# Kernel optimization log

Measured on AMD Instinct MI355X. Metric: run time of the kernel, lower is better.

## Reference

```python
import jax, jax.numpy as jnp
import numpy as np

B, N, D_MODEL, H = 2, 512, 256, 8
DH, DS, DE = 8, 8, 8          # hyperbolic / spherical / euclidean component dims
HEAD = D_MODEL // H           # 32
HALF = HEAD // 2              # 16 rope frequencies
KAPPA_S = 1.0                 # spherical curvature
EPS = 1e-6


def setup_inputs() -> dict:
    key = jax.random.key(0)
    ks = jax.random.split(key, 10)
    h = jax.random.normal(ks[0], (B, N, D_MODEL), jnp.float32)
    # manifold coords: hyperbolic part inside Poincare ball, spherical part on unit sphere
    xh = 0.3 * jnp.tanh(jax.random.normal(ks[1], (B, N, DH), jnp.float32))
    xs_raw = jax.random.normal(ks[2], (B, N, DS), jnp.float32)
    xs = xs_raw / jnp.linalg.norm(xs_raw, axis=-1, keepdims=True)
    xe = jax.random.normal(ks[3], (B, N, DE), jnp.float32)
    x = jnp.concatenate([xh, xs, xe], axis=-1)
    def lin(k):
        return 0.05 * jax.random.normal(k, (D_MODEL, D_MODEL), jnp.float32)
    inp = dict(
        h=h, x=x,
        Wq=lin(ks[4]), bq=jnp.zeros((D_MODEL,), jnp.float32),
        Wk=lin(ks[5]), bk=jnp.zeros((D_MODEL,), jnp.float32),
        Wv=lin(ks[6]), bv=jnp.zeros((D_MODEL,), jnp.float32),
        Wo=lin(ks[7]), bo=jnp.zeros((D_MODEL,), jnp.float32),
        w_kernel=jnp.ones((H, 3), jnp.float32),   # torch init: ones(num_heads, num_comp)
        beta=jnp.ones((H,), jnp.float32),
        edge_bias=0.1 * jax.random.normal(ks[8], (B, 1, N, N), jnp.float32),
        node_mask=jnp.ones((B, N), bool),
    )
    return inp


def _pairwise_geometry(x):
    """Returns dh (B,N,N), sdot (B,N,N), de2 (B,N,N), dist (B,N,N)."""
    xh, xs, xe = x[..., :DH], x[..., DH:DH + DS], x[..., DH + DS:]
    # hyperbolic: Poincare-ball distance arccosh(1 + 2|a-b|^2 / ((1-|a|^2)(1-|b|^2)))
    dh2_num = jnp.sum((xh[:, :, None, :] - xh[:, None, :, :]) ** 2, -1)
    one_m = 1.0 - jnp.sum(xh * xh, -1)                               # (B,N)
    arg = 1.0 + 2.0 * dh2_num / (one_m[:, :, None] * one_m[:, None, :])
    dh = jnp.arccosh(jnp.maximum(arg, 1.0 + EPS))
    # spherical: arccos of dot (unit vectors); raw dot kept for the kernel term
    sdot = jnp.einsum('bnd,bmd->bnm', xs, xs)
    ds = jnp.arccos(jnp.clip(sdot, -1.0 + EPS, 1.0 - EPS)) / np.sqrt(KAPPA_S)
    # euclidean: squared distance (kernel uses -d^2; product dist uses d^2)
    de2 = jnp.sum((xe[:, :, None, :] - xe[:, None, :, :]) ** 2, -1)
    dist = jnp.sqrt(dh * dh + ds * ds + de2)
    return dh, sdot, de2, dist


def reference(h, x, Wq, bq, Wk, bk, Wv, bv, Wo, bo, w_kernel, beta, edge_bias, node_mask):
    scale = 1.0 / np.sqrt(HEAD)
    rope_freq = jnp.exp(-np.log(10000.0) * jnp.arange(HALF, dtype=jnp.float32) / HALF)

    def heads(t):  # (B,N,D) -> (B,H,N,head)
        return t.reshape(B, N, H, HEAD).transpose(0, 2, 1, 3)

    Q = heads(h @ Wq.T + bq)
    K = heads(h @ Wk.T + bk)
    V = heads(h @ Wv.T + bv)

    dh, sdot, de2, dist = _pairwise_geometry(x)

    # M-RoPE: rotate Q by pairwise angle theta_ij = omega * d_M(x_i, x_j)
    theta = dist[..., None] * rope_freq                  # (B,N,N,half)
    cos_t = jnp.cos(theta)[:, None]                      # (B,1,N,N,half)
    sin_t = jnp.sin(theta)[:, None]
    q1, q2 = Q[..., 0::2], Q[..., 1::2]                  # (B,H,N,half)
    k1, k2 = K[..., 0::2], K[..., 1::2]
    qk_same = q1[:, :, :, None, :] * k1[:, :, None, :, :] + q2[:, :, :, None, :] * k2[:, :, None, :, :]
    qk_cross = q1[:, :, :, None, :] * k2[:, :, None, :, :] - q2[:, :, :, None, :] * k1[:, :, None, :, :]
    attn = (cos_t * qk_same + sin_t * qk_cross).sum(-1) * scale   # (B,H,N,N)

    # geodesic kernel bias: per-component kernels [H:-d_H, S:k*a.b, E:-|a-b|^2]
    kernel_stack = jnp.stack([-dh, KAPPA_S * sdot, -de2], axis=-1)  # (B,N,N,3)
    geo = jnp.einsum('hc,bnmc->bhnm', w_kernel, kernel_stack)
    attn = attn + beta[None, :, None, None] * geo + edge_bias

    attn = jnp.where(node_mask[:, None, None, :], attn, -jnp.inf)
    p = jax.nn.softmax(attn, axis=-1)
    out = jnp.einsum('bhnm,bhmd->bhnd', p, V).transpose(0, 2, 1, 3).reshape(B, N, D_MODEL)
    return out @ Wo.T + bo
```

## Files before the change

kernel.cpp:

```cpp
#include <hip/hip_runtime.h>

#define N_TOK 512
#define NH 8

typedef __attribute__((ext_vector_type(8))) short short8;
typedef __attribute__((ext_vector_type(4))) short short4v;
typedef __attribute__((ext_vector_type(4))) float f32x4;

__device__ __forceinline__ unsigned short f2bf(float f) {
    union { float f; unsigned u; } v; v.f = f;
    return (unsigned short)((v.u + 0x7FFF + ((v.u >> 16) & 1)) >> 16);
}

__global__ __launch_bounds__(256) void gemm_qkv_mfma(
    const float* __restrict__ A, const float* __restrict__ x,
    const float* __restrict__ Wq, const float* __restrict__ Wk, const float* __restrict__ Wv,
    const float* __restrict__ bq, const float* __restrict__ bk, const float* __restrict__ bv,
    float* __restrict__ Qb, float* __restrict__ KT, float* __restrict__ Vb,
    float* __restrict__ xT)
{
    const int bx = blockIdx.x;
    const int t = threadIdx.x;
    if (bx >= 768) {
        int idx = bx - 768;
        int b = idx / 24, k = idx % 24;
        const float* src = x + (size_t)b * 512 * 24 + k;
        float* dst = xT + (size_t)b * 12288 + k * 512;
        for (int j = t; j < 512; j += 256) dst[j] = src[j * 24];
        return;
    }
    const int z = bx >> 8, rem = bx & 255;
    const int m0 = (rem >> 3) * 32, n0 = (rem & 7) * 32;
    const float* W    = (z == 0) ? Wq : (z == 1) ? Wk : Wv;
    const float* bias = (z == 0) ? bq : (z == 1) ? bk : bv;

    __shared__ short As[32][264];
    __shared__ short Ws[32][264];

    #pragma unroll
    for (int r = 0; r < 8; ++r) {
        int idx = t + 256 * r;
        int row = idx >> 6, c4 = (idx & 63) * 4;
        float4 a = *(const float4*)&A[(m0 + row) * 256 + c4];
        short4v pa = {(short)f2bf(a.x), (short)f2bf(a.y), (short)f2bf(a.z), (short)f2bf(a.w)};
        *(short4v*)&As[row][c4] = pa;
        float4 w = *(const float4*)&W[(n0 + row) * 256 + c4];
        short4v pw = {(short)f2bf(w.x), (short)f2bf(w.y), (short)f2bf(w.z), (short)f2bf(w.w)};
        *(short4v*)&Ws[row][c4] = pw;
    }
    __syncthreads();

    const int w = t >> 6, lane = t & 63;
    const int wm = (w >> 1) * 16, wn = (w & 1) * 16;
    const int frow = lane & 15, kq = lane >> 4;

    f32x4 acc = {0.f, 0.f, 0.f, 0.f};
    #pragma unroll
    for (int k0 = 0; k0 < 8; ++k0) {
        short8 af = *(const short8*)&As[wm + frow][k0 * 32 + kq * 8];
        short8 wf = *(const short8*)&Ws[wn + frow][k0 * 32 + kq * 8];
        if (z == 1) acc = __builtin_amdgcn_mfma_f32_16x16x32_bf16(wf, af, acc, 0, 0, 0);
        else        acc = __builtin_amdgcn_mfma_f32_16x16x32_bf16(af, wf, acc, 0, 0, 0);
    }
    const int col = lane & 15, rq = (lane >> 4) * 4;
    if (z == 1) {
        int tok = m0 + wm + col;
        int bb = tok >> 9, jloc = tok & 511;
        #pragma unroll
        for (int r = 0; r < 4; ++r) {
            int d = n0 + wn + rq + r;
            KT[(size_t)bb * 131072 + d * 512 + jloc] = acc[r] + bias[d];
        }
    } else {
        float* C = (z == 0) ? Qb : Vb;
        float bsv = bias[n0 + wn + col];
        #pragma unroll
        for (int r = 0; r < 4; ++r)
            C[(m0 + wm + rq + r) * 256 + n0 + wn + col] = acc[r] + bsv;
    }
}

__global__ __launch_bounds__(512, 4) void attn_kernel(
    const float* __restrict__ Q, const float* __restrict__ KT, const float* __restrict__ V,
    const float* __restrict__ x, const float* __restrict__ xT,
    const float* __restrict__ wker, const float* __restrict__ beta,
    const float* __restrict__ eb, float* __restrict__ Ao)
{
    const int i0 = blockIdx.x * 2;
    const int b  = blockIdx.y;
    const int t  = threadIdx.x;
    const int lane = t & 63;
    const int h = __builtin_amdgcn_readfirstlane(t >> 6);

    __shared__ float csn[16][2][64][4];
    __shared__ float es[2][NH][128];
    __shared__ float gdh[2][128], gsd[2][128], gde[2][128];

    const float* q0p = Q + (size_t)(b * N_TOK + i0) * 256 + h * 32;
    const float* q1p = q0p + 256;
    const float wk0 = wker[h * 3 + 0], wk1 = wker[h * 3 + 1], wk2 = wker[h * 3 + 2];
    const float bet = beta[h];
    const float scale = 0.17677669529663687f;

    const int gjj = t & 127;
    const int gfh = __builtin_amdgcn_readfirstlane((t >> 7) & 1);
    const int gii = __builtin_amdgcn_readfirstlane(t >> 8);
    const float* xi = x + (size_t)(b * N_TOK + i0 + gii) * 24;
    float onemi = 1.0f;
    #pragma unroll
    for (int k = 0; k < 8; ++k) onemi -= xi[k] * xi[k];
    float frq[8];
    #pragma unroll
    for (int r = 0; r < 8; ++r)
        frq[r] = __expf(-0.5756462732485115f * (float)(gfh * 8 + r));

    float dsum[2] = {0.f, 0.f};
    float accv[2][4] = {{0.f,0.f,0.f,0.f},{0.f,0.f,0.f,0.f}};
    const int jsub = lane >> 3, dq = lane & 7;

    auto geom = [&](int tile) {
        const float* xc = xT + (size_t)b * 12288 + tile * 128 + gjj;
        float xv[24];
        #pragma unroll
        for (int k = 0; k < 24; ++k) xv[k] = xc[k * 512];
        float dh2 = 0.f, oj = 0.f, sd = 0.f, de2 = 0.f;
        #pragma unroll
        for (int k = 0; k < 8; ++k) { float d = xi[k] - xv[k]; dh2 += d * d; oj += xv[k] * xv[k]; }
        #pragma unroll
        for (int k = 0; k < 8; ++k) sd += xi[8 + k] * xv[8 + k];
        #pragma unroll
        for (int k = 0; k < 8; ++k) { float d = xi[16 + k] - xv[16 + k]; de2 += d * d; }
        float arg = 1.0f + 2.0f * dh2 / (onemi * (1.0f - oj));
        arg = fmaxf(arg, 1.0f + 1e-6f);
        float dh = __logf(arg + sqrtf(arg * arg - 1.0f));
        float sdc = fminf(fmaxf(sd, -1.0f + 1e-6f), 1.0f - 1e-6f);
        float dsp = acosf(sdc);
        float dist = sqrtf(dh * dh + dsp * dsp + de2);
        if (gfh == 0) { gdh[gii][gjj] = dh; gsd[gii][gjj] = sd; gde[gii][gjj] = de2; }
        #pragma unroll
        for (int r = 0; r < 8; ++r) {
            float sv, cv;
            __sincosf(dist * frq[r], &sv, &cv);
            *(float2*)&csn[gfh * 8 + r][gii][gjj >> 1][(gjj & 1) * 2] = make_float2(cv, sv);
        }
    };

    geom(0);
    __syncthreads();

    for (int tile = 0; tile < 4; ++tile) {
        {
            float dot[2][2] = {{0.f, 0.f}, {0.f, 0.f}};
            #pragma unroll
            for (int fg = 0; fg < 2; ++fg) {
                const float* kp = KT + (size_t)b * 131072 + (h * 32 + fg * 16) * 512
                                + tile * 128 + 2 * lane;
                float2 kv[16];
                #pragma unroll
                for (int cc = 0; cc < 16; ++cc) kv[cc] = *(const float2*)(kp + cc * 512);
                #pragma unroll
                for (int fl = 0; fl < 8; ++fl) {
                    const int f = fg * 8 + fl;
                    float2 k1 = kv[fl * 2], k2 = kv[fl * 2 + 1];
                    float q10 = q0p[f * 2], q20 = q0p[f * 2 + 1];
                    float q11 = q1p[f * 2], q21 = q1p[f * 2 + 1];
                    float4 c0 = *(const float4*)&csn[f][0][lane][0];
                    float4 c1 = *(const float4*)&csn[f][1][lane][0];
                    dot[0][0] += c0.x * (q10 * k1.x + q20 * k2.x) + c0.y * (q10 * k2.x - q20 * k1.x);
                    dot[0][1] += c0.z * (q10 * k1.y + q20 * k2.y) + c0.w * (q10 * k2.y - q20 * k1.y);
                    dot[1][0] += c1.x * (q11 * k1.x + q21 * k2.x) + c1.y * (q11 * k2.x - q21 * k1.x);
                    dot[1][1] += c1.z * (q11 * k1.y + q21 * k2.y) + c1.w * (q11 * k2.y - q21 * k1.y);
                }
            }
            #pragma unroll
            for (int ii = 0; ii < 2; ++ii) {
                float2 g1 = *(const float2*)&gdh[ii][2 * lane];
                float2 g2 = *(const float2*)&gsd[ii][2 * lane];
                float2 g3 = *(const float2*)&gde[ii][2 * lane];
                float2 e2 = *(const float2*)&eb[((size_t)b * N_TOK + i0 + ii) * N_TOK
                                                + tile * 128 + 2 * lane];
                float s0 = dot[ii][0] * scale + bet * (wk1 * g2.x - wk0 * g1.x - wk2 * g3.x) + e2.x;
                float s1 = dot[ii][1] * scale + bet * (wk1 * g2.y - wk0 * g1.y - wk2 * g3.y) + e2.y;
                float e0 = __expf(s0), e1 = __expf(s1);
                dsum[ii] += e0 + e1;
                *(float2*)&es[ii][h][2 * lane] = make_float2(e0, e1);
            }
        }
        __syncthreads();
        {
            const float* vp = V + (size_t)(b * N_TOK + tile * 128 + jsub) * 256 + h * 32 + dq * 4;
            #pragma unroll
            for (int it = 0; it < 16; ++it) {
                float4 v4 = *(const float4*)(vp + it * 8 * 256);
                int j = it * 8 + jsub;
                float e0 = es[0][h][j], e1 = es[1][h][j];
                accv[0][0] += e0 * v4.x; accv[0][1] += e0 * v4.y;
                accv[0][2] += e0 * v4.z; accv[0][3] += e0 * v4.w;
                accv[1][0] += e1 * v4.x; accv[1][1] += e1 * v4.y;
                accv[1][2] += e1 * v4.z; accv[1][3] += e1 * v4.w;
            }
        }
        if (tile < 3) geom(tile + 1);
        __syncthreads();
    }

    #pragma unroll
    for (int ii = 0; ii < 2; ++ii) {
        float v = dsum[ii];
        v += __shfl_xor(v, 1);  v += __shfl_xor(v, 2);  v += __shfl_xor(v, 4);
        v += __shfl_xor(v, 8);  v += __shfl_xor(v, 16); v += __shfl_xor(v, 32);
        dsum[ii] = 1.0f / v;
    }
    #pragma unroll
    for (int ii = 0; ii < 2; ++ii)
        #pragma unroll
        for (int dd = 0; dd < 4; ++dd) {
            float a = accv[ii][dd];
            a += __shfl_xor(a, 8); a += __shfl_xor(a, 16); a += __shfl_xor(a, 32);
            accv[ii][dd] = a;
        }
    if (jsub == 0) {
        #pragma unroll
        for (int ii = 0; ii < 2; ++ii) {
            float4 o;
            o.x = accv[ii][0] * dsum[ii]; o.y = accv[ii][1] * dsum[ii];
            o.z = accv[ii][2] * dsum[ii]; o.w = accv[ii][3] * dsum[ii];
            *(float4*)&Ao[(size_t)(b * N_TOK + i0 + ii) * 256 + h * 32 + dq * 4] = o;
        }
    }
}

__global__ __launch_bounds__(256) void gemm_out_mfma(
    const float* __restrict__ Ao, const float* __restrict__ Wo,
    const float* __restrict__ bo, float* __restrict__ out)
{
    const int t = threadIdx.x;
    const int m0 = (blockIdx.x >> 3) * 32, n0 = (blockIdx.x & 7) * 32;

    __shared__ short As[32][264];
    __shared__ short Ws[32][264];

    #pragma unroll
    for (int r = 0; r < 8; ++r) {
        int idx = t + 256 * r;
        int row = idx >> 6, c4 = (idx & 63) * 4;
        float4 a = *(const float4*)&Ao[(m0 + row) * 256 + c4];
        short4v pa = {(short)f2bf(a.x), (short)f2bf(a.y), (short)f2bf(a.z), (short)f2bf(a.w)};
        *(short4v*)&As[row][c4] = pa;
        float4 w = *(const float4*)&Wo[(n0 + row) * 256 + c4];
        short4v pw = {(short)f2bf(w.x), (short)f2bf(w.y), (short)f2bf(w.z), (short)f2bf(w.w)};
        *(short4v*)&Ws[row][c4] = pw;
    }
    __syncthreads();

    const int w = t >> 6, lane = t & 63;
    const int wm = (w >> 1) * 16, wn = (w & 1) * 16;
    const int frow = lane & 15, kq = lane >> 4;

    f32x4 acc = {0.f, 0.f, 0.f, 0.f};
    #pragma unroll
    for (int k0 = 0; k0 < 8; ++k0) {
        short8 af = *(const short8*)&As[wm + frow][k0 * 32 + kq * 8];
        short8 wf = *(const short8*)&Ws[wn + frow][k0 * 32 + kq * 8];
        acc = __builtin_amdgcn_mfma_f32_16x16x32_bf16(af, wf, acc, 0, 0, 0);
    }
    const int col = lane & 15, rq = (lane >> 4) * 4;
    float bsv = bo[n0 + wn + col];
    #pragma unroll
    for (int r = 0; r < 4; ++r)
        out[(m0 + wm + rq + r) * 256 + n0 + wn + col] = acc[r] + bsv;
}

extern "C" void kernel_launch(void* const* d_in, const int* in_sizes, int n_in,
                              void* d_out, int out_size, void* d_ws, size_t ws_size,
                              hipStream_t stream) {
    const float* hin  = (const float*)d_in[0];
    const float* x    = (const float*)d_in[1];
    const float* Wq   = (const float*)d_in[2];
    const float* bq   = (const float*)d_in[3];
    const float* Wk   = (const float*)d_in[4];
    const float* bk   = (const float*)d_in[5];
    const float* Wv   = (const float*)d_in[6];
    const float* bv   = (const float*)d_in[7];
    const float* Wo   = (const float*)d_in[8];
    const float* bo   = (const float*)d_in[9];
    const float* wker = (const float*)d_in[10];
    const float* beta = (const float*)d_in[11];
    const float* eb   = (const float*)d_in[12];
    float* out = (float*)d_out;
    float* w   = (float*)d_ws;

    float* Qb = w;
    float* KT = w + 262144;
    float* Vb = w + 524288;
    float* Ao = w + 786432;
    float* xT = w + 1048576;

    hipLaunchKernelGGL(gemm_qkv_mfma, dim3(816), dim3(256), 0, stream,
                       hin, x, Wq, Wk, Wv, bq, bk, bv, Qb, KT, Vb, xT);
    hipLaunchKernelGGL(attn_kernel, dim3(256, 2), dim3(512), 0, stream,
                       Qb, KT, Vb, x, xT, wker, beta, eb, Ao);
    hipLaunchKernelGGL(gemm_out_mfma, dim3(256), dim3(256), 0, stream,
                       Ao, Wo, bo, out);
}
```

Measured before the change: 135.0 us.

## Split pairwise geometry into separate kernel and make attention waves independent

Moves the per-pair manifold geometry (dh, sdot, de2, dist) into a new kernel that writes four B×N×N planes to the workspace. The attention kernel becomes wave-independent: each wave handles one (batch, head, row-pair), reads the precomputed geometry and computes its own sin/cos, with no block barriers. K is stored interleaved per frequency so each lane loads one float4. The previous design shared geometry and sincos across 8 heads in a block. Now each head redoes 16 sincos per pair and reads about 8 MB of extra geometry from global memory, trading block synchronisation for more transcendental work and memory traffic.

Result: slower. 138.0 us (+2.2%).

```diff
diff --git a/kernel.cpp b/kernel.cpp
--- a/kernel.cpp
+++ b/kernel.cpp
@@ -13,22 +13,13 @@
 }
 
 __global__ __launch_bounds__(256) void gemm_qkv_mfma(
-    const float* __restrict__ A, const float* __restrict__ x,
+    const float* __restrict__ A,
     const float* __restrict__ Wq, const float* __restrict__ Wk, const float* __restrict__ Wv,
     const float* __restrict__ bq, const float* __restrict__ bk, const float* __restrict__ bv,
-    float* __restrict__ Qb, float* __restrict__ KT, float* __restrict__ Vb,
-    float* __restrict__ xT)
+    float* __restrict__ Qb, float* __restrict__ KR, float* __restrict__ Vb)
 {
     const int bx = blockIdx.x;
     const int t = threadIdx.x;
-    if (bx >= 768) {
-        int idx = bx - 768;
-        int b = idx / 24, k = idx % 24;
-        const float* src = x + (size_t)b * 512 * 24 + k;
-        float* dst = xT + (size_t)b * 12288 + k * 512;
-        for (int j = t; j < 512; j += 256) dst[j] = src[j * 24];
-        return;
-    }
     const int z = bx >> 8, rem = bx & 255;
     const int m0 = (rem >> 3) * 32, n0 = (rem & 7) * 32;
     const float* W    = (z == 0) ? Wq : (z == 1) ? Wk : Wv;
@@ -65,11 +56,12 @@
     const int col = lane & 15, rq = (lane >> 4) * 4;
     if (z == 1) {
         int tok = m0 + wm + col;
-        int bb = tok >> 9, jloc = tok & 511;
+        int bb = tok >> 9, j = tok & 511;
         #pragma unroll
         for (int r = 0; r < 4; ++r) {
             int d = n0 + wn + rq + r;
-            KT[(size_t)bb * 131072 + d * 512 + jloc] = acc[r] + bias[d];
+            int h = d >> 5, dd = d & 31, f = dd >> 1, r2 = dd & 1;
+            KR[((size_t)bb * 128 + h * 16 + f) * 1024 + j * 2 + r2] = acc[r] + bias[d];
         }
     } else {
         float* C = (z == 0) ? Qb : Vb;
@@ -80,128 +72,150 @@
     }
 }
 
-__global__ __launch_bounds__(512, 4) void attn_kernel(
-    const float* __restrict__ Q, const float* __restrict__ KT, const float* __restrict__ V,
-    const float* __restrict__ x, const float* __restrict__ xT,
+__global__ __launch_bounds__(256) void geo_kernel(
+    const float* __restrict__ x, float* __restrict__ geo)
+{
+    const int j0 = blockIdx.x * 256;
+    const int i  = blockIdx.y;
+    const int b  = blockIdx.z;
+    const int t  = threadIdx.x;
+
+    __shared__ float xls[256 * 25];
+    const float4* xsrc = (const float4*)(x + ((size_t)b * N_TOK + j0) * 24);
+    #pragma unroll
+    for (int r = 0; r < 6; ++r) {
+        int idx = t + 256 * r;
+        float4 v = xsrc[idx];
+        int row = idx / 6, c = (idx % 6) * 4;
+        float* dst = &xls[row * 25 + c];
+        dst[0] = v.x; dst[1] = v.y; dst[2] = v.z; dst[3] = v.w;
+    }
+    const float* xi = x + ((size_t)b * N_TOK + i) * 24;
+    float onemi = 1.0f;
+    #pragma unroll
+    for (int k = 0; k < 8; ++k) onemi -= xi[k] * xi[k];
+    __syncthreads();
+
+    const float* xr = &xls[t * 25];
+    float dh2 = 0.f, oj = 0.f, sd = 0.f, de2 = 0.f;
+    #pragma unroll
+    for (int k = 0; k < 8; ++k) { float xj = xr[k]; float d = xi[k] - xj; dh2 += d * d; oj += xj * xj; }
+    #pragma unroll
+    for (int k = 0; k < 8; ++k) sd += xi[8 + k] * xr[8 + k];
+    #pragma unroll
+    for (int k = 0; k < 8; ++k) { float d = xi[16 + k] - xr[16 + k]; de2 += d * d; }
+    float arg = 1.0f + 2.0f * dh2 / (onemi * (1.0f - oj));
+    arg = fmaxf(arg, 1.0f + 1e-6f);
+    float dh = __logf(arg + sqrtf(arg * arg - 1.0f));
+    float sdc = fminf(fmaxf(sd, -1.0f + 1e-6f), 1.0f - 1e-6f);
+    float dsp = acosf(sdc);
+    float dist = sqrtf(dh * dh + dsp * dsp + de2);
+
+    size_t idx = ((size_t)b * N_TOK + i) * N_TOK + j0 + t;
+    geo[idx]               = dh;
+    geo[idx +     524288]  = sd;
+    geo[idx + 2 * 524288]  = de2;
+    geo[idx + 3 * 524288]  = dist;
+}
+
+__global__ __launch_bounds__(256, 4) void attn_kernel(
+    const float* __restrict__ Q, const float* __restrict__ KR, const float* __restrict__ V,
+    const float* __restrict__ geo, const float* __restrict__ eb,
     const float* __restrict__ wker, const float* __restrict__ beta,
-    const float* __restrict__ eb, float* __restrict__ Ao)
+    float* __restrict__ Ao)
 {
-    const int i0 = blockIdx.x * 2;
-    const int b  = blockIdx.y;
-    const int t  = threadIdx.x;
+    const float FRQ[16] = {
+        1.0f, 0.5623413251903491f, 0.31622776601683794f, 0.17782794100389228f,
+        0.1f, 0.05623413251903491f, 0.031622776601683794f, 0.017782794100389228f,
+        0.01f, 0.005623413251903491f, 0.0031622776601683794f, 0.0017782794100389228f,
+        0.001f, 0.0005623413251903491f, 0.00031622776601683795f, 0.00017782794100389228f};
+
+    const int t = threadIdx.x;
     const int lane = t & 63;
-    const int h = __builtin_amdgcn_readfirstlane(t >> 6);
-
-    __shared__ float csn[16][2][64][4];
-    __shared__ float es[2][NH][128];
-    __shared__ float gdh[2][128], gsd[2][128], gde[2][128];
-
-    const float* q0p = Q + (size_t)(b * N_TOK + i0) * 256 + h * 32;
+    const int wv = t >> 6;
+    const int wid = blockIdx.x * 4 + wv;
+    const int b  = __builtin_amdgcn_readfirstlane(wid >> 11);
+    const int h  = __builtin_amdgcn_readfirstlane((wid >> 8) & 7);
+    const int ip = __builtin_amdgcn_readfirstlane(wid & 255);
+    const int i0 = ip * 2;
+
+    __shared__ float es[4][2][128];
+
+    const float* q0p = Q + ((size_t)b * N_TOK + i0) * 256 + h * 32;
     const float* q1p = q0p + 256;
     const float wk0 = wker[h * 3 + 0], wk1 = wker[h * 3 + 1], wk2 = wker[h * 3 + 2];
     const float bet = beta[h];
     const float scale = 0.17677669529663687f;
 
-    const int gjj = t & 127;
-    const int gfh = __builtin_amdgcn_readfirstlane((t >> 7) & 1);
-    const int gii = __builtin_amdgcn_readfirstlane(t >> 8);
-    const float* xi = x + (size_t)(b * N_TOK + i0 + gii) * 24;
-    float onemi = 1.0f;
-    #pragma unroll
-    for (int k = 0; k < 8; ++k) onemi -= xi[k] * xi[k];
-    float frq[8];
-    #pragma unroll
-    for (int r = 0; r < 8; ++r)
-        frq[r] = __expf(-0.5756462732485115f * (float)(gfh * 8 + r));
+    const size_t gbase = ((size_t)b * N_TOK + i0) * N_TOK;
+    const float* kbase = KR + ((size_t)b * 128 + h * 16) * 1024;
 
     float dsum[2] = {0.f, 0.f};
-    float accv[2][4] = {{0.f,0.f,0.f,0.f},{0.f,0.f,0.f,0.f}};
+    float acc[2][4] = {{0.f,0.f,0.f,0.f},{0.f,0.f,0.f,0.f}};
     const int jsub = lane >> 3, dq = lane & 7;
 
-    auto geom = [&](int tile) {
-        const float* xc = xT + (size_t)b * 12288 + tile * 128 + gjj;
-        float xv[24];
-        #pragma unroll
-        for (int k = 0; k < 24; ++k) xv[k] = xc[k * 512];
-        float dh2 = 0.f, oj = 0.f, sd = 0.f, de2 = 0.f;
-        #pragma unroll
-        for (int k = 0; k < 8; ++k) { float d = xi[k] - xv[k]; dh2 += d * d; oj += xv[k] * xv[k]; }
-        #pragma unroll
-        for (int k = 0; k < 8; ++k) sd += xi[8 + k] * xv[8 + k];
-        #pragma unroll
-        for (int k = 0; k < 8; ++k) { float d = xi[16 + k] - xv[16 + k]; de2 += d * d; }
-        float arg = 1.0f + 2.0f * dh2 / (onemi * (1.0f - oj));
-        arg = fmaxf(arg, 1.0f + 1e-6f);
-        float dh = __logf(arg + sqrtf(arg * arg - 1.0f));
-        float sdc = fminf(fmaxf(sd, -1.0f + 1e-6f), 1.0f - 1e-6f);
-        float dsp = acosf(sdc);
-        float dist = sqrtf(dh * dh + dsp * dsp + de2);
-        if (gfh == 0) { gdh[gii][gjj] = dh; gsd[gii][gjj] = sd; gde[gii][gjj] = de2; }
-        #pragma unroll
-        for (int r = 0; r < 8; ++r) {
-            float sv, cv;
-            __sincosf(dist * frq[r], &sv, &cv);
-            *(float2*)&csn[gfh * 8 + r][gii][gjj >> 1][(gjj & 1) * 2] = make_float2(cv, sv);
-        }
-    };
-
-    geom(0);
-    __syncthreads();
-
     for (int tile = 0; tile < 4; ++tile) {
-        {
-            float dot[2][2] = {{0.f, 0.f}, {0.f, 0.f}};
+        const int j0 = tile * 128;
+        float2 gdh[2], gsd[2], gde[2], gds[2];
+        #pragma unroll
+        for (int ii = 0; ii < 2; ++ii) {
+            size_t gi = gbase + (size_t)ii * N_TOK + j0 + 2 * lane;
+            gdh[ii] = *(const float2*)&geo[gi];
+            gsd[ii] = *(const float2*)&geo[gi + 524288];
+            gde[ii] = *(const float2*)&geo[gi + 2 * 524288];
+            gds[ii] = *(const float2*)&geo[gi + 3 * 524288];
+        }
+        float dot[2][2] = {{0.f, 0.f}, {0.f, 0.f}};
+        #pragma unroll
+        for (int fg = 0; fg < 2; ++fg) {
+            float4 kv[8];
             #pragma unroll
-            for (int fg = 0; fg < 2; ++fg) {
-                const float* kp = KT + (size_t)b * 131072 + (h * 32 + fg * 16) * 512
-                                + tile * 128 + 2 * lane;
-                float2 kv[16];
+            for (int fl = 0; fl < 8; ++fl)
+                kv[fl] = *(const float4*)&kbase[(size_t)(fg * 8 + fl) * 1024 + (j0 + 2 * lane) * 2];
+            #pragma unroll
+            for (int fl = 0; fl < 8; ++fl) {
+                const int f = fg * 8 + fl;
+                const float frq = FRQ[f];
+                float4 kk = kv[fl];
                 #pragma unroll
-                for (int cc = 0; cc < 16; ++cc) kv[cc] = *(const float2*)(kp + cc * 512);
-                #pragma unroll
-                for (int fl = 0; fl < 8; ++fl) {
-                    const int f = fg * 8 + fl;
-                    float2 k1 = kv[fl * 2], k2 = kv[fl * 2 + 1];
-                    float q10 = q0p[f * 2], q20 = q0p[f * 2 + 1];
-                    float q11 = q1p[f * 2], q21 = q1p[f * 2 + 1];
-                    float4 c0 = *(const float4*)&csn[f][0][lane][0];
-                    float4 c1 = *(const float4*)&csn[f][1][lane][0];
-                    dot[0][0] += c0.x * (q10 * k1.x + q20 * k2.x) + c0.y * (q10 * k2.x - q20 * k1.x);
-                    dot[0][1] += c0.z * (q10 * k1.y + q20 * k2.y) + c0.w * (q10 * k2.y - q20 * k1.y);
-                    dot[1][0] += c1.x * (q11 * k1.x + q21 * k2.x) + c1.y * (q11 * k2.x - q21 * k1.x);
-                    dot[1][1] += c1.z * (q11 * k1.y + q21 * k2.y) + c1.w * (q11 * k2.y - q21 * k1.y);
+                for (int ii = 0; ii < 2; ++ii) {
+                    const float* qp = ii ? q1p : q0p;
+                    float q1 = qp[f * 2], q2 = qp[f * 2 + 1];
+                    float c0, s0, c1, s1;
+                    __sincosf(gds[ii].x * frq, &s0, &c0);
+                    __sincosf(gds[ii].y * frq, &s1, &c1);
+                    float t1 = q1 * kk.x + q2 * kk.y;
+                    float t2 = q1 * kk.y - q2 * kk.x;
+                    dot[ii][0] += c0 * t1 + s0 * t2;
+                    t1 = q1 * kk.z + q2 * kk.w;
+                    t2 = q1 * kk.w - q2 * kk.z;
+                    dot[ii][1] += c1 * t1 + s1 * t2;
                 }
             }
-            #pragma unroll
-            for (int ii = 0; ii < 2; ++ii) {
-                float2 g1 = *(const float2*)&gdh[ii][2 * lane];
-                float2 g2 = *(const float2*)&gsd[ii][2 * lane];
-                float2 g3 = *(const float2*)&gde[ii][2 * lane];
-                float2 e2 = *(const float2*)&eb[((size_t)b * N_TOK + i0 + ii) * N_TOK
-                                                + tile * 128 + 2 * lane];
-                float s0 = dot[ii][0] * scale + bet * (wk1 * g2.x - wk0 * g1.x - wk2 * g3.x) + e2.x;
-                float s1 = dot[ii][1] * scale + bet * (wk1 * g2.y - wk0 * g1.y - wk2 * g3.y) + e2.y;
-                float e0 = __expf(s0), e1 = __expf(s1);
-                dsum[ii] += e0 + e1;
-                *(float2*)&es[ii][h][2 * lane] = make_float2(e0, e1);
-            }
-        }
-        __syncthreads();
+        }
+        #pragma unroll
+        for (int ii = 0; ii < 2; ++ii) {
+            float2 e2 = *(const float2*)&eb[((size_t)b * N_TOK + i0 + ii) * N_TOK + j0 + 2 * lane];
+            float bias0 = bet * (wk1 * gsd[ii].x - wk0 * gdh[ii].x - wk2 * gde[ii].x) + e2.x;
+            float bias1 = bet * (wk1 * gsd[ii].y - wk0 * gdh[ii].y - wk2 * gde[ii].y) + e2.y;
+            float e0 = __expf(dot[ii][0] * scale + bias0);
+            float e1 = __expf(dot[ii][1] * scale + bias1);
+            dsum[ii] += e0 + e1;
+            *(float2*)&es[wv][ii][2 * lane] = make_float2(e0, e1);
+        }
         {
-            const float* vp = V + (size_t)(b * N_TOK + tile * 128 + jsub) * 256 + h * 32 + dq * 4;
+            const float* vp = V + ((size_t)b * N_TOK + j0 + jsub) * 256 + h * 32 + dq * 4;
             #pragma unroll
             for (int it = 0; it < 16; ++it) {
-                float4 v4 = *(const float4*)(vp + it * 8 * 256);
+                float4 v4 = *(const float4*)&vp[(size_t)it * 8 * 256];
                 int j = it * 8 + jsub;
-                float e0 = es[0][h][j], e1 = es[1][h][j];
-                accv[0][0] += e0 * v4.x; accv[0][1] += e0 * v4.y;
-                accv[0][2] += e0 * v4.z; accv[0][3] += e0 * v4.w;
-                accv[1][0] += e1 * v4.x; accv[1][1] += e1 * v4.y;
-                accv[1][2] += e1 * v4.z; accv[1][3] += e1 * v4.w;
+                float e0 = es[wv][0][j], e1 = es[wv][1][j];
+                acc[0][0] += e0 * v4.x; acc[0][1] += e0 * v4.y;
+                acc[0][2] += e0 * v4.z; acc[0][3] += e0 * v4.w;
+                acc[1][0] += e1 * v4.x; acc[1][1] += e1 * v4.y;
+                acc[1][2] += e1 * v4.z; acc[1][3] += e1 * v4.w;
             }
         }
-        if (tile < 3) geom(tile + 1);
-        __syncthreads();
     }
 
     #pragma unroll
@@ -215,17 +229,17 @@
     for (int ii = 0; ii < 2; ++ii)
         #pragma unroll
         for (int dd = 0; dd < 4; ++dd) {
-            float a = accv[ii][dd];
+            float a = acc[ii][dd];
             a += __shfl_xor(a, 8); a += __shfl_xor(a, 16); a += __shfl_xor(a, 32);
-            accv[ii][dd] = a;
+            acc[ii][dd] = a;
         }
     if (jsub == 0) {
         #pragma unroll
         for (int ii = 0; ii < 2; ++ii) {
             float4 o;
-            o.x = accv[ii][0] * dsum[ii]; o.y = accv[ii][1] * dsum[ii];
-            o.z = accv[ii][2] * dsum[ii]; o.w = accv[ii][3] * dsum[ii];
-            *(float4*)&Ao[(size_t)(b * N_TOK + i0 + ii) * 256 + h * 32 + dq * 4] = o;
+            o.x = acc[ii][0] * dsum[ii]; o.y = acc[ii][1] * dsum[ii];
+            o.z = acc[ii][2] * dsum[ii]; o.w = acc[ii][3] * dsum[ii];
+            *(float4*)&Ao[((size_t)b * N_TOK + i0 + ii) * 256 + h * 32 + dq * 4] = o;
         }
     }
 }
@@ -290,16 +304,18 @@
     float* out = (float*)d_out;
     float* w   = (float*)d_ws;
 
-    float* Qb = w;
-    float* KT = w + 262144;
-    float* Vb = w + 524288;
-    float* Ao = w + 786432;
-    float* xT = w + 1048576;
-
-    hipLaunchKernelGGL(gemm_qkv_mfma, dim3(816), dim3(256), 0, stream,
-                       hin, x, Wq, Wk, Wv, bq, bk, bv, Qb, KT, Vb, xT);
-    hipLaunchKernelGGL(attn_kernel, dim3(256, 2), dim3(512), 0, stream,
-                       Qb, KT, Vb, x, xT, wker, beta, eb, Ao);
+    float* Qb  = w;
+    float* KR  = w + 262144;
+    float* Vb  = w + 524288;
+    float* Ao  = w + 786432;
+    float* geo = w + 1048576;
+
+    hipLaunchKernelGGL(gemm_qkv_mfma, dim3(768), dim3(256), 0, stream,
+                       hin, Wq, Wk, Wv, bq, bk, bv, Qb, KR, Vb);
+    hipLaunchKernelGGL(geo_kernel, dim3(2, 512, 2), dim3(256), 0, stream,
+                       x, geo);
+    hipLaunchKernelGGL(attn_kernel, dim3(1024), dim3(256), 0, stream,
+                       Qb, KR, Vb, geo, eb, wker, beta, Ao);
     hipLaunchKernelGGL(gemm_out_mfma, dim3(256), dim3(256), 0, stream,
                        Ao, Wo, bo, out);
 }
```
